# Performance work log

Measured on AMD Instinct MI355X. Metric: run time of the kernel, lower is better.

## Reference

```python
import jax, jax.numpy as jnp
import numpy as np
from jax import lax

C64 = jnp.complex64

def _conv(x, w, b):
    y = lax.conv_general_dilated(x, w, (1, 1), 'SAME', dimension_numbers=('NCHW', 'OIHW', 'NCHW'))
    return y + b[None, :, None, None]

def _maxpool2(x):
    return lax.reduce_window(x, -jnp.inf, lax.max, (1, 1, 2, 2), (1, 1, 2, 2), 'VALID')

def _rx(t):
    c = jnp.cos(t / 2).astype(C64); s = jnp.sin(t / 2).astype(C64)
    return jnp.stack([jnp.stack([c, -1j * s], -1), jnp.stack([-1j * s, c], -1)], -2)

def _ry(t):
    c = jnp.cos(t / 2).astype(C64); s = jnp.sin(t / 2).astype(C64)
    return jnp.stack([jnp.stack([c, -s], -1), jnp.stack([s, c], -1)], -2)

def _rz(t):
    tc = t.astype(C64)
    em = jnp.exp(-0.5j * tc); ep = jnp.exp(0.5j * tc); z = jnp.zeros_like(em)
    return jnp.stack([jnp.stack([em, z], -1), jnp.stack([z, ep], -1)], -2)

_H = jnp.asarray((1.0 / np.sqrt(2.0)) * np.array([[1, 1], [1, -1]]), C64)
_SX = jnp.asarray(0.5 * np.array([[1 + 1j, 1 - 1j], [1 - 1j, 1 + 1j]]), C64)
_CNOT = jnp.asarray(np.array([[1, 0, 0, 0], [0, 1, 0, 0], [0, 0, 0, 1], [0, 0, 1, 0]]), C64)

def _apply1(state, U, w):
    # state: [B,2,2,2,2]; wire w lives on axis w+1. U: [2,2] or batched [B,2,2].
    s = jnp.moveaxis(state, w + 1, -1)
    if U.ndim == 3:
        s = jnp.einsum('bij,b...j->b...i', U, s)
    else:
        s = jnp.einsum('ij,b...j->b...i', U, s)
    return jnp.moveaxis(s, -1, w + 1)

def _apply2(state, U4, c, t):
    s = jnp.moveaxis(state, (c + 1, t + 1), (-2, -1))
    sh = s.shape
    s = s.reshape(sh[:-2] + (4,))
    s = jnp.einsum('ij,b...j->b...i', U4, s).reshape(sh)
    return jnp.moveaxis(s, (-2, -1), (c + 1, t + 1))

def _random_ops():
    # fixed instance of tq.RandomLayer(n_ops=30, wires=[0..3]), seed 42
    rng = np.random.default_rng(42)
    ops = []
    for _ in range(30):
        g = int(rng.integers(0, 4))
        if g == 3:
            w = rng.choice(4, size=2, replace=False)
            ops.append(('cnot', int(w[0]), int(w[1])))
        else:
            ops.append((['rx', 'ry', 'rz'][g], int(rng.integers(0, 4)), -1))
    return ops

_ROT = {'rx': _rx, 'ry': _ry, 'rz': _rz}

def _circuit(feat4, q_rx, q_ry, q_rz, rl_params):
    B = feat4.shape[0]
    state = jnp.zeros((B, 16), C64).at[:, 0].set(1.0).reshape(B, 2, 2, 2, 2)
    for i in range(4):  # RX encoding of the first 4 features
        state = _apply1(state, _rx(feat4[:, i]), i)
    for k, (name, a, b) in enumerate(_random_ops()):
        if name == 'cnot':
            state = _apply2(state, _CNOT, a, b)
        else:
            state = _apply1(state, _ROT[name](rl_params[k]), a)
    state = _apply1(state, _rx(q_rx[0]), 0)
    state = _apply1(state, _ry(q_ry[0]), 1)
    state = _apply1(state, _rz(q_rz[0]), 2)
    state = _apply2(state, _CNOT, 0, 3)
    state = _apply1(state, _H, 3)
    state = _apply1(state, _SX, 2)
    state = _apply2(state, _CNOT, 3, 0)
    p = state.real ** 2 + state.imag ** 2  # [B,2,2,2,2]
    z = jnp.array([1.0, -1.0], jnp.float32)
    exps = jnp.stack([jnp.tensordot(p.sum(axis=tuple(a for a in range(1, 5) if a != w + 1)), z, axes=1) for w in range(4)], axis=-1)
    return exps  # [B,4] Pauli-Z expectations

def _forward(x, conv1_w, conv1_b, conv2_w, conv2_b, fc_w, fc_b, q_rx, q_ry, q_rz, rl_params, bn_gamma, bn_beta, out_w, out_b):
    B = x.shape[0]
    h = jax.nn.relu(_conv(x, conv1_w, conv1_b)); h = _maxpool2(h)   # [B,8,14,14]
    h = jax.nn.relu(_conv(h, conv2_w, conv2_b)); h = _maxpool2(h)   # [B,16,7,7]
    feat = jax.nn.relu(h.reshape(B, -1) @ fc_w.T + fc_b)            # [B,64]
    exps = _circuit(feat[:, :4], q_rx, q_ry, q_rz, rl_params)       # [B,4]
    mean = exps.mean(0)
    var = ((exps - mean) ** 2).mean(0)  # biased var, training-mode BN
    y = (exps - mean) / jnp.sqrt(var + 1e-5) * bn_gamma + bn_beta
    return (y @ out_w.T + out_b)[:, 0]  # [B]

def setup_inputs() -> dict:
    key = jax.random.key(0)
    ks = jax.random.split(key, 16)
    B = 8192
    n = lambda k, sh, sc: jax.random.normal(k, sh, jnp.float32) * sc
    return {
        'x': jax.random.normal(ks[0], (B, 1, 28, 28), jnp.float32),
        'conv1_w': n(ks[1], (8, 1, 3, 3), 0.3),
        'conv1_b': n(ks[2], (8,), 0.1),
        'conv2_w': n(ks[3], (16, 8, 3, 3), 0.2),
        'conv2_b': n(ks[4], (16,), 0.1),
        'fc_w': n(ks[5], (64, 784), 0.05),
        'fc_b': n(ks[6], (64,), 0.1),
        'q_rx': n(ks[7], (1,), 1.0),
        'q_ry': n(ks[8], (1,), 1.0),
        'q_rz': n(ks[9], (1,), 1.0),
        'rl_params': jax.random.uniform(ks[10], (30,), jnp.float32, 0.0, 2.0 * np.pi),
        'bn_gamma': jnp.ones((4,), jnp.float32),
        'bn_beta': jnp.zeros((4,), jnp.float32),
        'out_w': n(ks[11], (1, 4), 0.5),
        'out_b': n(ks[12], (1,), 0.1),
    }

def reference(x, conv1_w, conv1_b, conv2_w, conv2_b, fc_w, fc_b, q_rx, q_ry, q_rz, rl_params, bn_gamma, bn_beta, out_w, out_b):
    return _forward(x, conv1_w, conv1_b, conv2_w, conv2_b, fc_w, fc_b, q_rx, q_ry, q_rz, rl_params, bn_gamma, bn_beta, out_w, out_b)
```

## Files before the change

kernel.cpp:

```cpp
#include <hip/hip_runtime.h>
#include <stdint.h>
#include <math.h>

#define NOPS 37

struct Ops37 {
    int type[NOPS];
    int a[NOPS];
    int b[NOPS];
};

static void build_ops_host(Ops37* ops) {
    uint32_t pool[4];
    uint32_t hc = 0x43b0d7e5u;
    auto hmix = [&hc](uint32_t value) -> uint32_t {
        value ^= hc;
        hc *= 0x931e8875u;
        value *= hc;
        value ^= value >> 16;
        return value;
    };
    auto mixf = [](uint32_t x, uint32_t y) -> uint32_t {
        uint32_t r = (x * 0xca01f9ddu) - (y * 0x4973f715u);
        r ^= r >> 16;
        return r;
    };
    pool[0] = hmix(42u);
    for (int i = 1; i < 4; i++) pool[i] = hmix(0u);
    for (int s = 0; s < 4; s++)
        for (int d = 0; d < 4; d++)
            if (s != d) pool[d] = mixf(pool[d], hmix(pool[s]));

    uint32_t st[8];
    {
        uint32_t hcb = 0x8b51f9ddu;
        for (int i = 0; i < 8; i++) {
            uint32_t dv = pool[i & 3];
            dv ^= hcb;
            hcb *= 0x58f38dedu;
            dv *= hcb;
            dv ^= dv >> 16;
            st[i] = dv;
        }
    }
    typedef __uint128_t u128;
    const uint64_t v0 = (uint64_t)st[0] | ((uint64_t)st[1] << 32);
    const uint64_t v1 = (uint64_t)st[2] | ((uint64_t)st[3] << 32);
    const uint64_t v2 = (uint64_t)st[4] | ((uint64_t)st[5] << 32);
    const uint64_t v3 = (uint64_t)st[6] | ((uint64_t)st[7] << 32);
    const u128 initstate = (((u128)v0) << 64) | v1;
    const u128 initseq   = (((u128)v2) << 64) | v3;
    const u128 MULT = (((u128)0x2360ed051fc65da4ULL) << 64) | 0x4385df649fccf645ULL;

    u128 state = 0;
    const u128 inc = (initseq << 1) | 1;
    state = state * MULT + inc;
    state += initstate;
    state = state * MULT + inc;

    bool has32 = false;
    uint32_t cached = 0;
    auto next64 = [&]() -> uint64_t {
        state = state * MULT + inc;
        uint64_t hi = (uint64_t)(state >> 64);
        uint64_t lo = (uint64_t)state;
        unsigned rot = (unsigned)(state >> 122) & 63u;
        uint64_t v = hi ^ lo;
        return (v >> rot) | (v << ((64u - rot) & 63u));
    };
    auto next32 = [&]() -> uint32_t {
        if (has32) { has32 = false; return cached; }
        uint64_t n = next64();
        has32 = true;
        cached = (uint32_t)(n >> 32);
        return (uint32_t)n;
    };
    auto lem = [&](uint32_t rng) -> uint32_t {
        const uint32_t rng_excl = rng + 1u;
        uint64_t m = (uint64_t)next32() * (uint64_t)rng_excl;
        uint32_t leftover = (uint32_t)m;
        if (leftover < rng_excl) {
            const uint32_t threshold = (0xFFFFFFFFu - rng) % rng_excl;
            while (leftover < threshold) {
                m = (uint64_t)next32() * (uint64_t)rng_excl;
                leftover = (uint32_t)m;
            }
        }
        return (uint32_t)(m >> 32);
    };

    for (int k = 0; k < 30; k++) {
        uint32_t g = lem(3);
        if (g == 3u) {
            uint32_t i0 = lem(2);
            uint32_t vv = lem(3);
            uint32_t i1 = (vv == i0) ? 3u : vv;
            uint32_t j = lem(1);
            if (j == 0u) { uint32_t t = i0; i0 = i1; i1 = t; }
            ops->type[k] = 3; ops->a[k] = (int)i0; ops->b[k] = (int)i1;
        } else {
            uint32_t w = lem(3);
            ops->type[k] = (int)g; ops->a[k] = (int)w; ops->b[k] = -1;
        }
    }
    ops->type[30] = 0; ops->a[30] = 0; ops->b[30] = -1;
    ops->type[31] = 1; ops->a[31] = 1; ops->b[31] = -1;
    ops->type[32] = 2; ops->a[32] = 2; ops->b[32] = -1;
    ops->type[33] = 3; ops->a[33] = 0; ops->b[33] = 3;
    ops->type[34] = 4; ops->a[34] = 3; ops->b[34] = -1;
    ops->type[35] = 5; ops->a[35] = 2; ops->b[35] = -1;
    ops->type[36] = 3; ops->a[36] = 3; ops->b[36] = 0;
}

__global__ __launch_bounds__(64) void build_u_kernel(
        const float* __restrict__ rl, const float* __restrict__ qrx,
        const float* __restrict__ qry, const float* __restrict__ qrz,
        float* __restrict__ Uout, Ops37 ops) {
    int j = threadIdx.x;
    if (j >= 16) return;
    double cr[16], ci[16];
    for (int i = 0; i < 16; i++) { cr[i] = (i == j) ? 1.0 : 0.0; ci[i] = 0.0; }
    for (int k = 0; k < NOPS; k++) {
        int t = ops.type[k];
        if (t == 3) {
            int mc = 8 >> ops.a[k], mt = 8 >> ops.b[k];
            for (int i = 0; i < 16; i++) {
                if ((i & mc) && !(i & mt)) {
                    int i2 = i | mt;
                    double tr = cr[i], ti = ci[i];
                    cr[i] = cr[i2]; ci[i] = ci[i2];
                    cr[i2] = tr;    ci[i2] = ti;
                }
            }
        } else {
            double g00r, g00i, g01r, g01i, g10r, g10i, g11r, g11i;
            if (t == 4) {
                const double r = 0.70710678118654752440;
                g00r = r; g00i = 0; g01r = r;  g01i = 0;
                g10r = r; g10i = 0; g11r = -r; g11i = 0;
            } else if (t == 5) {
                g00r = 0.5; g00i = 0.5;  g01r = 0.5; g01i = -0.5;
                g10r = 0.5; g10i = -0.5; g11r = 0.5; g11i = 0.5;
            } else {
                float th = (k < 30) ? rl[k]
                         : (k == 30 ? qrx[0] : (k == 31 ? qry[0] : qrz[0]));
                double c = cos(0.5 * (double)th), s = sin(0.5 * (double)th);
                if (t == 0) {
                    g00r = c; g00i = 0;  g01r = 0; g01i = -s;
                    g10r = 0; g10i = -s; g11r = c; g11i = 0;
                } else if (t == 1) {
                    g00r = c; g00i = 0; g01r = -s; g01i = 0;
                    g10r = s; g10i = 0; g11r = c;  g11i = 0;
                } else {
                    g00r = c; g00i = -s; g01r = 0; g01i = 0;
                    g10r = 0; g10i = 0;  g11r = c; g11i = s;
                }
            }
            int m = 8 >> ops.a[k];
            for (int i = 0; i < 16; i++) {
                if (!(i & m)) {
                    int i2 = i | m;
                    double ar = cr[i], ai = ci[i], br = cr[i2], bi = ci[i2];
                    cr[i]  = g00r * ar - g00i * ai + g01r * br - g01i * bi;
                    ci[i]  = g00r * ai + g00i * ar + g01r * bi + g01i * br;
                    cr[i2] = g10r * ar - g10i * ai + g11r * br - g11i * bi;
                    ci[i2] = g10r * ai + g10i * ar + g11r * bi + g11i * br;
                }
            }
        }
    }
    for (int i = 0; i < 16; i++) {
        Uout[2 * (i * 16 + j)]     = (float)cr[i];
        Uout[2 * (i * 16 + j) + 1] = (float)ci[i];
    }
}

#define XPo   0
#define H2o   0
#define H1o   1020
#define REDo  3868
#define FEATo 3876
#define PSIo  3880
#define PVo   3912
#define SMSZ  3928

#define H1CS  356
#define H1RS  22

__global__ __launch_bounds__(128) void fused_fwd_kernel(
        const float* __restrict__ x,
        const float* __restrict__ c1w, const float* __restrict__ c1b,
        const float* __restrict__ c2w, const float* __restrict__ c2b,
        const float* __restrict__ fcw, const float* __restrict__ fcb,
        const float* __restrict__ Ug, float* __restrict__ exps) {
    __shared__ __align__(16) float SM[SMSZ];
    const int tid = threadIdx.x;
    const int bidx = blockIdx.x;

    {
        const float* xb = x + (size_t)bidx * 784;
        for (int i = tid; i < 1020; i += 128) {
            int r = i / 34, c = i - r * 34;
            float v = 0.f;
            if (r >= 1 && r <= 28 && c >= 1 && c <= 28) v = xb[(r - 1) * 28 + (c - 1)];
            SM[XPo + i] = v;
        }
    }
    for (int i = tid; i < 8 * H1CS; i += 128) SM[H1o + i] = 0.f;
    __syncthreads();

    {
        const int c    = tid & 7;
        const int pos0 = tid >> 3;
        float wv[9];
        #pragma unroll
        for (int t = 0; t < 9; t++) wv[t] = c1w[c * 9 + t];
        const float bb = c1b[c];
        for (int pos = pos0; pos < 98; pos += 16) {
            int py = pos / 7, pxp = pos - py * 7;
            float P[4][6];
            #pragma unroll
            for (int r = 0; r < 4; r++) {
                const float2 a  = *(const float2*)&SM[XPo + (2 * py + r) * 34 + 4 * pxp];
                const float2 b_ = *(const float2*)&SM[XPo + (2 * py + r) * 34 + 4 * pxp + 2];
                const float2 c_ = *(const float2*)&SM[XPo + (2 * py + r) * 34 + 4 * pxp + 4];
                P[r][0] = a.x; P[r][1] = a.y; P[r][2] = b_.x;
                P[r][3] = b_.y; P[r][4] = c_.x; P[r][5] = c_.y;
            }
            #pragma unroll
            for (int half = 0; half < 2; half++) {
                float m = -3.4e38f;
                #pragma unroll
                for (int dy = 0; dy < 2; dy++)
                    #pragma unroll
                    for (int dx = 0; dx < 2; dx++) {
                        float acc = 0.f;
                        #pragma unroll
                        for (int ky = 0; ky < 3; ky++)
                            #pragma unroll
                            for (int kx = 0; kx < 3; kx++)
                                acc = fmaf(P[dy + ky][2 * half + dx + kx], wv[ky * 3 + kx], acc);
                        m = fmaxf(m, acc);
                    }
                SM[H1o + c * H1CS + (py + 1) * H1RS + (2 * pxp + half + 1)] = fmaxf(m + bb, 0.f);
            }
        }
    }
    __syncthreads();

    if (tid < 112) {
        int c2 = tid / 7, py = tid - (tid / 7) * 7;
        float acc[7][4];
        #pragma unroll
        for (int px = 0; px < 7; px++)
            #pragma unroll
            for (int s = 0; s < 4; s++) acc[px][s] = 0.f;
        for (int c1 = 0; c1 < 8; c1++) {
            float R[4][16];
            #pragma unroll
            for (int r = 0; r < 4; r++) {
                #pragma unroll
                for (int q = 0; q < 8; q++) {
                    const float2 v = *(const float2*)&SM[H1o + c1 * H1CS + (2 * py + r) * H1RS + 2 * q];
                    R[r][2 * q] = v.x; R[r][2 * q + 1] = v.y;
                }
            }
            float w[9];
            #pragma unroll
            for (int t = 0; t < 9; t++) w[t] = c2w[(c2 * 8 + c1) * 9 + t];
            #pragma unroll
            for (int px = 0; px < 7; px++)
                #pragma unroll
                for (int dy = 0; dy < 2; dy++)
                    #pragma unroll
                    for (int dx = 0; dx < 2; dx++) {
                        float a = acc[px][dy * 2 + dx];
                        #pragma unroll
                        for (int ky = 0; ky < 3; ky++)
                            #pragma unroll
                            for (int kx = 0; kx < 3; kx++)
                                a = fmaf(R[dy + ky][2 * px + dx + kx], w[ky * 3 + kx], a);
                        acc[px][dy * 2 + dx] = a;
                    }
        }
        const float bb = c2b[c2];
        #pragma unroll
        for (int px = 0; px < 7; px++) {
            float m = fmaxf(fmaxf(acc[px][0], acc[px][1]), fmaxf(acc[px][2], acc[px][3]));
            SM[H2o + c2 * 49 + py * 7 + px] = fmaxf(m + bb, 0.f);
        }
    }
    __syncthreads();

    {
        float a0 = 0.f, a1 = 0.f, a2 = 0.f, a3 = 0.f;
        for (int j = tid; j < 784; j += 128) {
            float h = SM[H2o + j];
            a0 = fmaf(h, fcw[j],        a0);
            a1 = fmaf(h, fcw[784 + j],  a1);
            a2 = fmaf(h, fcw[1568 + j], a2);
            a3 = fmaf(h, fcw[2352 + j], a3);
        }
        #pragma unroll
        for (int off = 32; off > 0; off >>= 1) {
            a0 += __shfl_down(a0, off);
            a1 += __shfl_down(a1, off);
            a2 += __shfl_down(a2, off);
            a3 += __shfl_down(a3, off);
        }
        if ((tid & 63) == 0) {
            int wid = tid >> 6;
            SM[REDo + wid * 4 + 0] = a0;
            SM[REDo + wid * 4 + 1] = a1;
            SM[REDo + wid * 4 + 2] = a2;
            SM[REDo + wid * 4 + 3] = a3;
        }
    }
    __syncthreads();
    if (tid < 4)
        SM[FEATo + tid] = fmaxf(SM[REDo + tid] + SM[REDo + 4 + tid] + fcb[tid], 0.f);
    __syncthreads();

    if (tid < 16) {
        int j = tid;
        float re = 1.f, im = 0.f;
        #pragma unroll
        for (int w = 0; w < 4; w++) {
            float half = 0.5f * SM[FEATo + w];
            float cc = cosf(half), ss = sinf(half);
            if ((j >> (3 - w)) & 1) {
                float nr = ss * im, ni = -ss * re;
                re = nr; im = ni;
            } else {
                re *= cc; im *= cc;
            }
        }
        SM[PSIo + 2 * j] = re; SM[PSIo + 2 * j + 1] = im;
    }
    __syncthreads();
    if (tid < 16) {
        int r = tid;
        float ar = 0.f, ai = 0.f;
        const float2* U2 = (const float2*)Ug;
        #pragma unroll
        for (int j2 = 0; j2 < 16; j2++) {
            float2 u = U2[r * 16 + j2];
            float pr = SM[PSIo + 2 * j2], pi = SM[PSIo + 2 * j2 + 1];
            ar += u.x * pr - u.y * pi;
            ai += u.x * pi + u.y * pr;
        }
        SM[PVo + r] = ar * ar + ai * ai;
    }
    __syncthreads();
    if (tid < 4) {
        int w = tid, msk = 8 >> w;
        float e = 0.f;
        #pragma unroll
        for (int r = 0; r < 16; r++) {
            float p = SM[PVo + r];
            e += (r & msk) ? -p : p;
        }
        exps[(size_t)bidx * 4 + w] = e;
    }
}

__global__ __launch_bounds__(256) void bn_stats_kernel(
        const float* __restrict__ exps, const float* __restrict__ gamma,
        const float* __restrict__ beta, const float* __restrict__ ow,
        const float* __restrict__ ob, float* __restrict__ stats, int B) {
    int tid = threadIdx.x;
    double s0 = 0, s1 = 0, s2 = 0, s3 = 0, q0 = 0, q1 = 0, q2 = 0, q3 = 0;
    for (int i = tid; i < B; i += 256) {
        float4 e = reinterpret_cast<const float4*>(exps)[i];
        s0 += e.x; q0 += (double)e.x * e.x;
        s1 += e.y; q1 += (double)e.y * e.y;
        s2 += e.z; q2 += (double)e.z * e.z;
        s3 += e.w; q3 += (double)e.w * e.w;
    }
    __shared__ double red[8][256];
    red[0][tid] = s0; red[1][tid] = s1; red[2][tid] = s2; red[3][tid] = s3;
    red[4][tid] = q0; red[5][tid] = q1; red[6][tid] = q2; red[7][tid] = q3;
    __syncthreads();
    for (int st = 128; st > 0; st >>= 1) {
        if (tid < st)
            for (int k = 0; k < 8; k++) red[k][tid] += red[k][tid + st];
        __syncthreads();
    }
    if (tid == 0) {
        double C = (double)ob[0];
        for (int w = 0; w < 4; w++) {
            double mean = red[w][0] / (double)B;
            double var  = red[4 + w][0] / (double)B - mean * mean;
            double inv  = 1.0 / sqrt(var + 1e-5);
            double scale = (double)gamma[w] * inv;
            stats[w] = (float)(scale * (double)ow[w]);
            C += ((double)beta[w] - mean * scale) * (double)ow[w];
        }
        stats[4] = (float)C;
    }
}

__global__ __launch_bounds__(256) void out_kernel(
        const float* __restrict__ exps, const float* __restrict__ stats,
        float* __restrict__ out, int B) {
    int b = blockIdx.x * 256 + threadIdx.x;
    if (b >= B) return;
    float4 e = reinterpret_cast<const float4*>(exps)[b];
    out[b] = fmaf(e.x, stats[0],
             fmaf(e.y, stats[1],
             fmaf(e.z, stats[2],
             fmaf(e.w, stats[3], stats[4]))));
}

extern "C" void kernel_launch(void* const* d_in, const int* in_sizes, int n_in,
                              void* d_out, int out_size, void* d_ws, size_t ws_size,
                              hipStream_t stream) {
    const float* x   = (const float*)d_in[0];
    const float* c1w = (const float*)d_in[1];
    const float* c1b = (const float*)d_in[2];
    const float* c2w = (const float*)d_in[3];
    const float* c2b = (const float*)d_in[4];
    const float* fcw = (const float*)d_in[5];
    const float* fcb = (const float*)d_in[6];
    const float* qrx = (const float*)d_in[7];
    const float* qry = (const float*)d_in[8];
    const float* qrz = (const float*)d_in[9];
    const float* rl  = (const float*)d_in[10];
    const float* gmm = (const float*)d_in[11];
    const float* bta = (const float*)d_in[12];
    const float* ow  = (const float*)d_in[13];
    const float* ob  = (const float*)d_in[14];
    float* out = (float*)d_out;
    const int B = in_sizes[0] / 784;
    if (B <= 0) return;

    Ops37 ops;
    build_ops_host(&ops);

    float* ws    = (float*)d_ws;
    float* U     = ws;
    float* exps  = ws + 512;
    float* stats = ws + 512 + 4 * (size_t)B;

    build_u_kernel<<<dim3(1), dim3(64), 0, stream>>>(rl, qrx, qry, qrz, U, ops);
    fused_fwd_kernel<<<dim3(B), dim3(128), 0, stream>>>(
        x, c1w, c1b, c2w, c2b, fcw, fcb, U, exps);
    bn_stats_kernel<<<dim3(1), dim3(256), 0, stream>>>(exps, gmm, bta, ow, ob, stats, B);
    out_kernel<<<dim3((B + 255) / 256), dim3(256), 0, stream>>>(exps, stats, out, B);
}
```

Before: 179.2 us.

## Switch unitary build to fp32, shrink H1 padding, fuse BN stats with output

The 16x16 circuit unitary is now built in single precision instead of double, which removes slow FP64 work in a serial one-block kernel. The padded shared-memory buffer for the first conv output is shrunk (smaller row and channel strides), and only its border cells are zeroed instead of the whole buffer. The batch-norm statistics kernel now also writes the final output, so the separate output kernel and its launch are removed. In exchange the unitary carries fp32 rounding error, and the final 8192-element output pass runs on a single 256-thread block.

```diff
diff --git a/kernel.cpp b/kernel.cpp
--- a/kernel.cpp
+++ b/kernel.cpp
@@ -118,8 +118,8 @@
         float* __restrict__ Uout, Ops37 ops) {
     int j = threadIdx.x;
     if (j >= 16) return;
-    double cr[16], ci[16];
-    for (int i = 0; i < 16; i++) { cr[i] = (i == j) ? 1.0 : 0.0; ci[i] = 0.0; }
+    float cr[16], ci[16];
+    for (int i = 0; i < 16; i++) { cr[i] = (i == j) ? 1.f : 0.f; ci[i] = 0.f; }
     for (int k = 0; k < NOPS; k++) {
         int t = ops.type[k];
         if (t == 3) {
@@ -127,24 +127,24 @@
             for (int i = 0; i < 16; i++) {
                 if ((i & mc) && !(i & mt)) {
                     int i2 = i | mt;
-                    double tr = cr[i], ti = ci[i];
+                    float tr = cr[i], ti = ci[i];
                     cr[i] = cr[i2]; ci[i] = ci[i2];
                     cr[i2] = tr;    ci[i2] = ti;
                 }
             }
         } else {
-            double g00r, g00i, g01r, g01i, g10r, g10i, g11r, g11i;
+            float g00r, g00i, g01r, g01i, g10r, g10i, g11r, g11i;
             if (t == 4) {
-                const double r = 0.70710678118654752440;
+                const float r = 0.70710678118654752440f;
                 g00r = r; g00i = 0; g01r = r;  g01i = 0;
                 g10r = r; g10i = 0; g11r = -r; g11i = 0;
             } else if (t == 5) {
-                g00r = 0.5; g00i = 0.5;  g01r = 0.5; g01i = -0.5;
-                g10r = 0.5; g10i = -0.5; g11r = 0.5; g11i = 0.5;
+                g00r = 0.5f; g00i = 0.5f;  g01r = 0.5f; g01i = -0.5f;
+                g10r = 0.5f; g10i = -0.5f; g11r = 0.5f; g11i = 0.5f;
             } else {
                 float th = (k < 30) ? rl[k]
                          : (k == 30 ? qrx[0] : (k == 31 ? qry[0] : qrz[0]));
-                double c = cos(0.5 * (double)th), s = sin(0.5 * (double)th);
+                float c = cosf(0.5f * th), s = sinf(0.5f * th);
                 if (t == 0) {
                     g00r = c; g00i = 0;  g01r = 0; g01i = -s;
                     g10r = 0; g10i = -s; g11r = c; g11i = 0;
@@ -160,7 +160,7 @@
             for (int i = 0; i < 16; i++) {
                 if (!(i & m)) {
                     int i2 = i | m;
-                    double ar = cr[i], ai = ci[i], br = cr[i2], bi = ci[i2];
+                    float ar = cr[i], ai = ci[i], br = cr[i2], bi = ci[i2];
                     cr[i]  = g00r * ar - g00i * ai + g01r * br - g01i * bi;
                     ci[i]  = g00r * ai + g00i * ar + g01r * bi + g01i * br;
                     cr[i2] = g10r * ar - g10i * ai + g11r * br - g11i * bi;
@@ -170,22 +170,22 @@
         }
     }
     for (int i = 0; i < 16; i++) {
-        Uout[2 * (i * 16 + j)]     = (float)cr[i];
-        Uout[2 * (i * 16 + j) + 1] = (float)ci[i];
+        Uout[2 * (i * 16 + j)]     = cr[i];
+        Uout[2 * (i * 16 + j) + 1] = ci[i];
     }
 }
 
 #define XPo   0
 #define H2o   0
 #define H1o   1020
-#define REDo  3868
-#define FEATo 3876
-#define PSIo  3880
-#define PVo   3912
-#define SMSZ  3928
-
-#define H1CS  356
-#define H1RS  22
+#define REDo  3356
+#define FEATo 3364
+#define PSIo  3368
+#define PVo   3400
+#define SMSZ  3416
+
+#define H1CS  292
+#define H1RS  18
 
 __global__ __launch_bounds__(128) void fused_fwd_kernel(
         const float* __restrict__ x,
@@ -206,7 +206,14 @@
             SM[XPo + i] = v;
         }
     }
-    for (int i = tid; i < 8 * H1CS; i += 128) SM[H1o + i] = 0.f;
+    for (int i = tid; i < 480; i += 128) {
+        int ch = i / 60, j = i - ch * 60;
+        int row, col;
+        if (j < 16)      { row = 0;  col = j; }
+        else if (j < 32) { row = 15; col = j - 16; }
+        else             { row = 1 + ((j - 32) >> 1); col = ((j - 32) & 1) * 15; }
+        SM[H1o + ch * H1CS + row * H1RS + col] = 0.f;
+    }
     __syncthreads();
 
     {
@@ -364,10 +371,10 @@
     }
 }
 
-__global__ __launch_bounds__(256) void bn_stats_kernel(
+__global__ __launch_bounds__(256) void bn_out_kernel(
         const float* __restrict__ exps, const float* __restrict__ gamma,
         const float* __restrict__ beta, const float* __restrict__ ow,
-        const float* __restrict__ ob, float* __restrict__ stats, int B) {
+        const float* __restrict__ ob, float* __restrict__ out, int B) {
     int tid = threadIdx.x;
     double s0 = 0, s1 = 0, s2 = 0, s3 = 0, q0 = 0, q1 = 0, q2 = 0, q3 = 0;
     for (int i = tid; i < B; i += 256) {
@@ -378,6 +385,7 @@
         s3 += e.w; q3 += (double)e.w * e.w;
     }
     __shared__ double red[8][256];
+    __shared__ float stats_s[5];
     red[0][tid] = s0; red[1][tid] = s1; red[2][tid] = s2; red[3][tid] = s3;
     red[4][tid] = q0; red[5][tid] = q1; red[6][tid] = q2; red[7][tid] = q3;
     __syncthreads();
@@ -393,23 +401,18 @@
             double var  = red[4 + w][0] / (double)B - mean * mean;
             double inv  = 1.0 / sqrt(var + 1e-5);
             double scale = (double)gamma[w] * inv;
-            stats[w] = (float)(scale * (double)ow[w]);
+            stats_s[w] = (float)(scale * (double)ow[w]);
             C += ((double)beta[w] - mean * scale) * (double)ow[w];
         }
-        stats[4] = (float)C;
-    }
-}
-
-__global__ __launch_bounds__(256) void out_kernel(
-        const float* __restrict__ exps, const float* __restrict__ stats,
-        float* __restrict__ out, int B) {
-    int b = blockIdx.x * 256 + threadIdx.x;
-    if (b >= B) return;
-    float4 e = reinterpret_cast<const float4*>(exps)[b];
-    out[b] = fmaf(e.x, stats[0],
-             fmaf(e.y, stats[1],
-             fmaf(e.z, stats[2],
-             fmaf(e.w, stats[3], stats[4]))));
+        stats_s[4] = (float)C;
+    }
+    __syncthreads();
+    const float A0 = stats_s[0], A1 = stats_s[1], A2 = stats_s[2],
+                A3 = stats_s[3], Cc = stats_s[4];
+    for (int b = tid; b < B; b += 256) {
+        float4 e = reinterpret_cast<const float4*>(exps)[b];
+        out[b] = fmaf(e.x, A0, fmaf(e.y, A1, fmaf(e.z, A2, fmaf(e.w, A3, Cc))));
+    }
 }
 
 extern "C" void kernel_launch(void* const* d_in, const int* in_sizes, int n_in,
@@ -437,14 +440,12 @@
     Ops37 ops;
     build_ops_host(&ops);
 
-    float* ws    = (float*)d_ws;
-    float* U     = ws;
-    float* exps  = ws + 512;
-    float* stats = ws + 512 + 4 * (size_t)B;
+    float* ws   = (float*)d_ws;
+    float* U    = ws;
+    float* exps = ws + 512;
 
     build_u_kernel<<<dim3(1), dim3(64), 0, stream>>>(rl, qrx, qry, qrz, U, ops);
     fused_fwd_kernel<<<dim3(B), dim3(128), 0, stream>>>(
         x, c1w, c1b, c2w, c2b, fcw, fcb, U, exps);
-    bn_stats_kernel<<<dim3(1), dim3(256), 0, stream>>>(exps, gmm, bta, ow, ob, stats, B);
-    out_kernel<<<dim3((B + 255) / 256), dim3(256), 0, stream>>>(exps, stats, out, B);
+    bn_out_kernel<<<dim3(1), dim3(256), 0, stream>>>(exps, gmm, bta, ow, ob, out, B);
 }
```

Result: faster. 153.8 us (-14.2%).
